# Performance work log

Hardware: AMD Instinct MI355X
Metric: run time of the kernel (lower is better)

Reference implementation:

```python
import jax, jax.numpy as jnp
import numpy as np
import math

B, S, D, H = 2, 2048, 1024, 16
DK = D // H


def setup_inputs() -> dict:
    key = jax.random.key(0)
    ks = jax.random.split(key, 11)
    f = jnp.float32
    return {
        "query": jax.random.normal(ks[0], (B, S, D), f),
        "key": jax.random.normal(ks[1], (B, S, D), f),
        "value": jax.random.normal(ks[2], (B, S, D), f),
        "wq": jax.random.normal(ks[3], (D, D), f) * 0.02,
        "bq": jnp.zeros((D,), f),
        "wk": jax.random.normal(ks[4], (D, D), f) * 0.02,
        "bk": jnp.zeros((D,), f),
        "wv": jax.random.normal(ks[5], (D, D), f) * 0.02,
        "bv": jnp.zeros((D,), f),
        "wo": jax.random.normal(ks[6], (D, D), f) * 0.02,
        "bo": jnp.zeros((D,), f),
    }


def reference(query, key, value, wq, bq, wk, bk, wv, bv, wo, bo):
    # Linear projections (torch Linear: y = x @ W.T + b)
    q = query @ wq.T + bq
    k = key @ wk.T + bk
    v = value @ wv.T + bv
    # [B,S,D] -> [B,H,S,DK]
    q = q.reshape(B, S, H, DK).transpose(0, 2, 1, 3)
    k = k.reshape(B, S, H, DK).transpose(0, 2, 1, 3)
    v = v.reshape(B, S, H, DK).transpose(0, 2, 1, 3)
    scores = jnp.einsum("bhqd,bhkd->bhqk", q, k) / math.sqrt(DK)
    causal = jnp.triu(jnp.ones((S, S), dtype=bool), k=1)  # strict upper triangle masked
    scores = jnp.where(causal, -jnp.inf, scores)
    attn = jax.nn.softmax(scores, axis=-1)  # dropout is identity in eval (p=0)
    x = jnp.einsum("bhqk,bhkd->bhqd", attn, v)
    x = x.transpose(0, 2, 1, 3).reshape(B, S, D)
    return x @ wo.T + bo
```

## Files before the change

### kernel.cpp

```cpp
#include <hip/hip_runtime.h>
#include <math.h>

#define BB 2
#define SS 2048
#define DD 1024
#define HH 16
#define DKK 64
#define MM (BB * SS)
#define KK DD
#define VSTR 2176

typedef __attribute__((ext_vector_type(8))) short short8;
typedef __attribute__((ext_vector_type(4))) float floatx4;

__device__ inline unsigned short f2bf(float x) {
    unsigned int u = __float_as_uint(x);
    u += 0x7fffu + ((u >> 16) & 1u);
    return (unsigned short)(u >> 16);
}

__device__ inline unsigned int pkbf(float a, float b) {
    return (__float_as_uint(b) & 0xffff0000u) | (__float_as_uint(a) >> 16);
}

__device__ inline void cast4f(const float* __restrict__ in, unsigned short* __restrict__ out, int i) {
    const float4 v = *(const float4*)(in + i);
    unsigned long long pk = (unsigned long long)f2bf(v.x)
                          | ((unsigned long long)f2bf(v.y) << 16)
                          | ((unsigned long long)f2bf(v.z) << 32)
                          | ((unsigned long long)f2bf(v.w) << 48);
    *(unsigned long long*)(out + i) = pk;
}

__global__ __launch_bounds__(256) void cast_all(const float* __restrict__ q, const float* __restrict__ k,
                                                const float* __restrict__ v,
                                                const float* __restrict__ wq, const float* __restrict__ wk,
                                                const float* __restrict__ wv, const float* __restrict__ wo,
                                                unsigned short* __restrict__ oq, unsigned short* __restrict__ ok,
                                                unsigned short* __restrict__ ov,
                                                unsigned short* __restrict__ owq, unsigned short* __restrict__ owk,
                                                unsigned short* __restrict__ owv, unsigned short* __restrict__ owo) {
    const int blk = blockIdx.x;
    const float* in;
    unsigned short* out;
    int idx;
    if (blk < 12288) {
        const int w = blk >> 12;
        idx = blk & 4095;
        in  = (w == 0) ? q : (w == 1) ? k : v;
        out = (w == 0) ? oq : (w == 1) ? ok : ov;
    } else {
        const int w = (blk - 12288) >> 10;
        idx = (blk - 12288) & 1023;
        in  = (w == 0) ? wq : (w == 1) ? wk : (w == 2) ? wv : wo;
        out = (w == 0) ? owq : (w == 1) ? owk : (w == 2) ? owv : owo;
    }
    cast4f(in, out, (idx * 256 + threadIdx.x) * 4);
}

#define GLDS(gp, lp) __builtin_amdgcn_global_load_lds( \
    (const __attribute__((address_space(1))) void*)(gp), \
    (__attribute__((address_space(3))) void*)(lp), 16, 0, 0)

#define SCHED0() __builtin_amdgcn_sched_barrier(0)
#define BAR()    __builtin_amdgcn_s_barrier()
#define WAITL0() asm volatile("s_waitcnt lgkmcnt(0)" ::: "memory")
#define WAITV(n) asm volatile("s_waitcnt vmcnt(" #n ")" ::: "memory")

template<int MT>
__device__ __forceinline__ void gemm_mainloop(const unsigned short* __restrict__ A,
                                              const unsigned short* __restrict__ W,
                                              int m0, int n0,
                                              unsigned short* __restrict__ As,
                                              unsigned short* __restrict__ Bs,
                                              floatx4 (&acc)[MT * 4][4]) {
    const int t    = threadIdx.x;
    const int lane = t & 63;
    const int wave = t >> 6;
    const int col  = lane & 15;
    const int quad = lane >> 4;
    const int wr   = wave >> 2;
    const int wc   = wave & 3;
    const int wm   = wr * (MT * 64);
    const int wn   = wc * 64;

    const int r   = t >> 3;
    const int cs  = t & 7;
    const int ksw = (cs ^ (r & 7)) * 8;

    const int sA0 = (quad ^ (col & 7)) * 8;
    const int sA1 = ((quad + 4) ^ (col & 7)) * 8;

    auto stage = [&](int kt, int pb) {
        const int k0 = kt * 64;
        #pragma unroll
        for (int g = 0; g < 2 * MT; ++g)
            GLDS(A + (size_t)(m0 + g * 64 + r) * KK + k0 + ksw,
                 &As[pb * (MT * 128 * 64) + (g * 64 + r) * 64 + cs * 8]);
        #pragma unroll
        for (int g = 0; g < 4; ++g)
            GLDS(W + (size_t)(n0 + g * 64 + r) * KK + k0 + ksw,
                 &Bs[pb * (256 * 64) + (g * 64 + r) * 64 + cs * 8]);
    };

    stage(0, 0);
    stage(1, 1);
    if constexpr (MT == 2) { WAITV(8); } else { WAITV(6); }
    SCHED0(); BAR(); SCHED0();

    const int NK = KK / 64;
    for (int kt = 0; kt < NK; ++kt) {
        const int p = kt & 1;
        const unsigned short* Ab = &As[p * (MT * 128 * 64)];
        const unsigned short* Bb = &Bs[p * (256 * 64)];

        short8 a0[MT * 4], a1[MT * 4], b0[4], b1[4];
        #pragma unroll
        for (int i = 0; i < MT * 4; ++i) {
            const unsigned short* ar = Ab + (wm + i * 16 + col) * 64;
            a0[i] = *(const short8*)(ar + sA0);
            a1[i] = *(const short8*)(ar + sA1);
        }
        #pragma unroll
        for (int j = 0; j < 4; ++j) {
            const unsigned short* br = Bb + (wn + j * 16 + col) * 64;
            b0[j] = *(const short8*)(br + sA0);
            b1[j] = *(const short8*)(br + sA1);
        }

        #pragma unroll
        for (int i = 0; i < MT * 4; ++i)
            #pragma unroll
            for (int j = 0; j < 4; ++j)
                acc[i][j] = __builtin_amdgcn_mfma_f32_16x16x32_bf16(a0[i], b0[j], acc[i][j], 0, 0, 0);

        WAITL0(); SCHED0();
        BAR(); SCHED0();

        if (kt + 2 < NK) stage(kt + 2, p);

        __builtin_amdgcn_s_setprio(1);
        #pragma unroll
        for (int i = 0; i < MT * 4; ++i)
            #pragma unroll
            for (int j = 0; j < 4; ++j)
                acc[i][j] = __builtin_amdgcn_mfma_f32_16x16x32_bf16(a1[i], b1[j], acc[i][j], 0, 0, 0);
        __builtin_amdgcn_s_setprio(0);

        if (kt + 2 < NK) {
            if constexpr (MT == 2) { WAITV(8); } else { WAITV(6); }
        } else {
            WAITV(0);
        }
        SCHED0(); BAR(); SCHED0();
    }
}

__global__ __launch_bounds__(512, 2) void gemm_qkv(const unsigned short* __restrict__ qB,
                                                   const unsigned short* __restrict__ kB,
                                                   const unsigned short* __restrict__ vB,
                                                   const unsigned short* __restrict__ wqB,
                                                   const unsigned short* __restrict__ wkB,
                                                   const unsigned short* __restrict__ wvB,
                                                   const float* __restrict__ bq,
                                                   const float* __restrict__ bk,
                                                   const float* __restrict__ bv,
                                                   unsigned short* __restrict__ Qh,
                                                   unsigned short* __restrict__ Kh,
                                                   unsigned short* __restrict__ Vt) {
    __shared__ __align__(16) unsigned short As[2 * 256 * 64];
    __shared__ __align__(16) unsigned short Bs[2 * 256 * 64];

    const int bid   = blockIdx.x;
    const int wgid  = (bid & 7) * 24 + (bid >> 3);
    const int which = wgid >> 6;
    const int tile  = wgid & 63;
    const int m0    = (tile & 15) * 256;
    const int n0    = (tile >> 4) * 256;

    const unsigned short* A = (which == 0) ? qB : (which == 1) ? kB : vB;
    const unsigned short* W = (which == 0) ? wqB : (which == 1) ? wkB : wvB;
    const float* bias       = (which == 0) ? bq : (which == 1) ? bk : bv;

    floatx4 acc[8][4] = {};
    gemm_mainloop<2>(A, W, m0, n0, As, Bs, acc);

    const int t    = threadIdx.x;
    const int lane = t & 63;
    const int wave = t >> 6;
    const int col  = lane & 15;
    const int quad = lane >> 4;
    const int wm   = (wave >> 2) * 128;
    const int wn   = (wave & 3) * 64;

    #pragma unroll
    for (int i = 0; i < 8; ++i) {
        #pragma unroll
        for (int j = 0; j < 4; ++j) {
            const int n  = n0 + wn + j * 16 + col;
            const float bv0 = bias[n];
            const int h = n >> 6, dk = n & 63;
            const int mb  = m0 + wm + i * 16 + quad * 4;
            const int bdx = mb >> 11, s = mb & 2047;
            if (which != 2) {
                unsigned short* O = (which == 0) ? Qh : Kh;
                #pragma unroll
                for (int rr = 0; rr < 4; ++rr)
                    O[(((size_t)(bdx * HH + h)) * SS + (s + rr)) * DKK + dk] = f2bf(acc[i][j][rr] + bv0);
            } else {
                unsigned short* vp = Vt + (((size_t)(bdx * HH + h)) * DKK + dk) * VSTR + s;
                uint2 w;
                w.x = (unsigned int)f2bf(acc[i][j][0] + bv0) | ((unsigned int)f2bf(acc[i][j][1] + bv0) << 16);
                w.y = (unsigned int)f2bf(acc[i][j][2] + bv0) | ((unsigned int)f2bf(acc[i][j][3] + bv0) << 16);
                *(uint2*)vp = w;
            }
        }
    }
}

__global__ __launch_bounds__(512, 2) void gemm_out(const unsigned short* __restrict__ A,
                                                   const unsigned short* __restrict__ W,
                                                   const float* __restrict__ bias,
                                                   float* __restrict__ C) {
    __shared__ __align__(16) unsigned short As[2 * 128 * 64];
    __shared__ __align__(16) unsigned short Bs[2 * 256 * 64];

    const int bid  = blockIdx.x;
    const int wgid = (bid & 7) * 16 + (bid >> 3);
    const int m0   = (wgid & 31) * 128;
    const int n0   = (wgid >> 5) * 256;

    floatx4 acc[4][4] = {};
    gemm_mainloop<1>(A, W, m0, n0, As, Bs, acc);

    const int t    = threadIdx.x;
    const int lane = t & 63;
    const int wave = t >> 6;
    const int col  = lane & 15;
    const int quad = lane >> 4;
    const int wm   = (wave >> 2) * 64;
    const int wn   = (wave & 3) * 64;

    #pragma unroll
    for (int i = 0; i < 4; ++i) {
        #pragma unroll
        for (int j = 0; j < 4; ++j) {
            const int n = n0 + wn + j * 16 + col;
            const float bv0 = bias[n];
            #pragma unroll
            for (int rr = 0; rr < 4; ++rr) {
                const int m = m0 + wm + i * 16 + quad * 4 + rr;
                C[(size_t)m * DD + n] = acc[i][j][rr] + bv0;
            }
        }
    }
}

#define C1 0.18033688011112042f
#define C2 11.541560327111707f
#define MFMA __builtin_amdgcn_mfma_f32_16x16x32_bf16

__global__ __launch_bounds__(512) void attn_mfma(const unsigned short* __restrict__ Qh,
                                                 const unsigned short* __restrict__ Kh,
                                                 const unsigned short* __restrict__ Vt,
                                                 unsigned short* __restrict__ X) {
    __shared__ __align__(16) unsigned short Ks[2][64 * 64];
    __shared__ __align__(16) unsigned short Vs[2][64 * 64];
    __shared__ __align__(16) unsigned short Plds[8][16 * 40];

    const int t    = threadIdx.x;
    const int lane = t & 63;
    const int wave = t >> 6;
    const int col  = lane & 15;
    const int quad = lane >> 4;

    const int lin = blockIdx.x;
    const int bh  = (lin & 7) + 8 * ((lin >> 3) & 3);
    const int pr  = lin >> 5;
    const int b   = bh / HH, h = bh % HH;

    const int cX  = (wave < 4) ? (31 - pr) : pr;
    const int q0  = cX * 64 + (wave & 3) * 16;
    const int nst = 32 - pr;

    const unsigned short* Kb = Kh + (size_t)bh * SS * DKK;
    const unsigned short* Vb = Vt + (size_t)bh * DKK * VSTR;

    const int r0  = t >> 3;
    const int sg0 = ((t & 7) ^ (r0 & 7)) * 8;

    unsigned short* Pw = &Plds[wave][0];

    const unsigned short* Qb = Qh + ((size_t)bh * SS + q0) * DKK;
    const short8 qa0 = *(const short8*)(Qb + (size_t)col * DKK + quad * 8);
    const short8 qa1 = *(const short8*)(Qb + (size_t)col * DKK + 32 + quad * 8);

    floatx4 o0 = {0.f, 0.f, 0.f, 0.f}, o1 = o0, o2 = o0, o3 = o0;
    float lp = 0.f;

    const int ksA = ((quad)      ^ (col & 7)) * 8;
    const int ksB = ((quad | 4)  ^ (col & 7)) * 8;

    GLDS(Kb + (size_t)r0 * DKK + sg0,  &Ks[0][t * 8]);
    GLDS(Vb + (size_t)r0 * VSTR + sg0, &Vs[0][t * 8]);

    int cur = 0;
    for (int kb = 0; kb < nst; ++kb) {
        __syncthreads();

        if (kb + 1 < nst) {
            const int jn = (kb + 1) * 64;
            const int nx = cur ^ 1;
            GLDS(Kb + (size_t)(jn + r0) * DKK + sg0,  &Ks[nx][t * 8]);
            GLDS(Vb + (size_t)r0 * VSTR + jn + sg0,   &Vs[nx][t * 8]);
        }

        const unsigned short* Kp = &Ks[cur][0];
        const unsigned short* Vp = &Vs[cur][0];

        #pragma unroll
        for (int hh = 0; hh < 2; ++hh) {
            const int j0 = kb * 64 + hh * 32;
            if (j0 < q0 + 16) {
                const short8 k0 = *(const short8*)(Kp + (hh * 32 + col) * 64 + ksA);
                const short8 k1 = *(const short8*)(Kp + (hh * 32 + col) * 64 + ksB);
                const short8 k2 = *(const short8*)(Kp + (hh * 32 + col + 16) * 64 + ksA);
                const short8 k3 = *(const short8*)(Kp + (hh * 32 + col + 16) * 64 + ksB);

                floatx4 t0 = {0.f, 0.f, 0.f, 0.f}, t1 = t0;
                __builtin_amdgcn_s_setprio(1);
                t0 = MFMA(k0, qa0, t0, 0, 0, 0);
                t0 = MFMA(k1, qa1, t0, 0, 0, 0);
                t1 = MFMA(k2, qa0, t1, 0, 0, 0);
                t1 = MFMA(k3, qa1, t1, 0, 0, 0);
                __builtin_amdgcn_s_setprio(0);

                float p[8];
                if (j0 + 31 > q0) {
                    const int lim = q0 + col - j0;
                    #pragma unroll
                    for (int r = 0; r < 4; ++r) {
                        p[r]     = (quad * 4 + r      <= lim) ? __builtin_exp2f(fmaf(t0[r], C1, -C2)) : 0.f;
                        p[4 + r] = (16 + quad * 4 + r <= lim) ? __builtin_exp2f(fmaf(t1[r], C1, -C2)) : 0.f;
                    }
                } else {
                    #pragma unroll
                    for (int r = 0; r < 4; ++r) {
                        p[r]     = __builtin_exp2f(fmaf(t0[r], C1, -C2));
                        p[4 + r] = __builtin_exp2f(fmaf(t1[r], C1, -C2));
                    }
                }
                lp += (p[0] + p[1]) + (p[2] + p[3]) + (p[4] + p[5]) + (p[6] + p[7]);

                uint2 w0 = { pkbf(p[0], p[1]), pkbf(p[2], p[3]) };
                uint2 w1 = { pkbf(p[4], p[5]), pkbf(p[6], p[7]) };
                *(uint2*)(Pw + col * 40 + quad * 4)      = w0;
                *(uint2*)(Pw + col * 40 + 16 + quad * 4) = w1;

                const short8 pb = *(const short8*)(Pw + col * 40 + quad * 8);
                const int vs = hh ? ksB : ksA;
                const short8 v0 = *(const short8*)(Vp + (col)      * 64 + vs);
                const short8 v1 = *(const short8*)(Vp + (col + 16) * 64 + vs);
                const short8 v2 = *(const short8*)(Vp + (col + 32) * 64 + vs);
                const short8 v3 = *(const short8*)(Vp + (col + 48) * 64 + vs);
                __builtin_amdgcn_s_setprio(1);
                o0 = MFMA(v0, pb, o0, 0, 0, 0);
                o1 = MFMA(v1, pb, o1, 0, 0, 0);
                o2 = MFMA(v2, pb, o2, 0, 0, 0);
                o3 = MFMA(v3, pb, o3, 0, 0, 0);
                __builtin_amdgcn_s_setprio(0);
            }
        }

        cur ^= 1;
    }

    lp += __shfl_xor(lp, 16, 64);
    lp += __shfl_xor(lp, 32, 64);
    const float li = 1.f / lp;

    unsigned short* Xp = X + ((size_t)(b * SS + q0 + col)) * DD + h * DKK + quad * 4;
    {
        uint2 w;
        w.x = (unsigned int)f2bf(o0[0] * li) | ((unsigned int)f2bf(o0[1] * li) << 16);
        w.y = (unsigned int)f2bf(o0[2] * li) | ((unsigned int)f2bf(o0[3] * li) << 16);
        *(uint2*)(Xp + 0) = w;
        w.x = (unsigned int)f2bf(o1[0] * li) | ((unsigned int)f2bf(o1[1] * li) << 16);
        w.y = (unsigned int)f2bf(o1[2] * li) | ((unsigned int)f2bf(o1[3] * li) << 16);
        *(uint2*)(Xp + 16) = w;
        w.x = (unsigned int)f2bf(o2[0] * li) | ((unsigned int)f2bf(o2[1] * li) << 16);
        w.y = (unsigned int)f2bf(o2[2] * li) | ((unsigned int)f2bf(o2[3] * li) << 16);
        *(uint2*)(Xp + 32) = w;
        w.x = (unsigned int)f2bf(o3[0] * li) | ((unsigned int)f2bf(o3[1] * li) << 16);
        w.y = (unsigned int)f2bf(o3[2] * li) | ((unsigned int)f2bf(o3[3] * li) << 16);
        *(uint2*)(Xp + 48) = w;
    }
}

extern "C" void kernel_launch(void* const* d_in, const int* in_sizes, int n_in,
                              void* d_out, int out_size, void* d_ws, size_t ws_size,
                              hipStream_t stream) {
    const float* query = (const float*)d_in[0];
    const float* key   = (const float*)d_in[1];
    const float* value = (const float*)d_in[2];
    const float* wq    = (const float*)d_in[3];
    const float* bq    = (const float*)d_in[4];
    const float* wk    = (const float*)d_in[5];
    const float* bk    = (const float*)d_in[6];
    const float* wv    = (const float*)d_in[7];
    const float* bv    = (const float*)d_in[8];
    const float* wo    = (const float*)d_in[9];
    const float* bo    = (const float*)d_in[10];

    char* ws = (char*)d_ws;
    const size_t MB = 1024 * 1024;
    unsigned short* qB  = (unsigned short*)(ws);
    unsigned short* kB  = (unsigned short*)(ws + 8 * MB);
    unsigned short* vB  = (unsigned short*)(ws + 16 * MB);
    unsigned short* wqB = (unsigned short*)(ws + 24 * MB);
    unsigned short* wkB = (unsigned short*)(ws + 26 * MB);
    unsigned short* wvB = (unsigned short*)(ws + 28 * MB);
    unsigned short* woB = (unsigned short*)(ws + 30 * MB);
    unsigned short* Qh  = (unsigned short*)(ws + 32 * MB);
    unsigned short* Kh  = (unsigned short*)(ws + 40 * MB);
    unsigned short* Vt  = (unsigned short*)(ws + 48 * MB);
    unsigned short* Xb  = qB;

    cast_all<<<16384, 256, 0, stream>>>(query, key, value, wq, wk, wv, wo,
                                        qB, kB, vB, wqB, wkB, wvB, woB);

    gemm_qkv<<<192, 512, 0, stream>>>(qB, kB, vB, wqB, wkB, wvB, bq, bk, bv, Qh, Kh, Vt);

    attn_mfma<<<512, 512, 0, stream>>>(Qh, Kh, Vt, Xb);

    gemm_out<<<128, 512, 0, stream>>>(Xb, woB, bo, (float*)d_out);
}
```

Measured before the change: 219.2 us.

## Shrink GEMM tiles to 128x128 with 256-thread blocks and grid-stride cast

Replaces the 256x256 / 128x256 GEMM tiles with a uniform 128x128 tile run by 4 waves, raising block counts (768 for QKV, 256 for output) to fill more CUs. The pipeline changes from a two-stage-ahead prefetch with a mid-iteration barrier to a single prefetch per iteration followed by a full vmcnt(0) wait. The cast kernel becomes a grid-stride loop with 8 items per thread over 2048 blocks. Smaller tiles lower per-block operand reuse and the simpler pipeline may expose more load latency.

```diff
diff --git a/kernel.cpp b/kernel.cpp
--- a/kernel.cpp
+++ b/kernel.cpp
@@ -40,22 +40,27 @@
                                                 unsigned short* __restrict__ ov,
                                                 unsigned short* __restrict__ owq, unsigned short* __restrict__ owk,
                                                 unsigned short* __restrict__ owv, unsigned short* __restrict__ owo) {
-    const int blk = blockIdx.x;
-    const float* in;
-    unsigned short* out;
-    int idx;
-    if (blk < 12288) {
-        const int w = blk >> 12;
-        idx = blk & 4095;
-        in  = (w == 0) ? q : (w == 1) ? k : v;
-        out = (w == 0) ? oq : (w == 1) ? ok : ov;
-    } else {
-        const int w = (blk - 12288) >> 10;
-        idx = (blk - 12288) & 1023;
-        in  = (w == 0) ? wq : (w == 1) ? wk : (w == 2) ? wv : wo;
-        out = (w == 0) ? owq : (w == 1) ? owk : (w == 2) ? owv : owo;
-    }
-    cast4f(in, out, (idx * 256 + threadIdx.x) * 4);
+    const int tid = blockIdx.x * 256 + threadIdx.x;
+    #pragma unroll
+    for (int it = 0; it < 8; ++it) {
+        const int g = tid + it * 524288;
+        const float* in;
+        unsigned short* out;
+        int idx;
+        if (g < 3145728) {
+            const int w = g >> 20;
+            idx = g & 1048575;
+            in  = (w == 0) ? q : (w == 1) ? k : v;
+            out = (w == 0) ? oq : (w == 1) ? ok : ov;
+        } else {
+            const int gw = g - 3145728;
+            const int w = gw >> 18;
+            idx = gw & 262143;
+            in  = (w == 0) ? wq : (w == 1) ? wk : (w == 2) ? wv : wo;
+            out = (w == 0) ? owq : (w == 1) ? owk : (w == 2) ? owv : owo;
+        }
+        cast4f(in, out, idx * 4);
+    }
 }
 
 #define GLDS(gp, lp) __builtin_amdgcn_global_load_lds( \
@@ -67,26 +72,22 @@
 #define WAITL0() asm volatile("s_waitcnt lgkmcnt(0)" ::: "memory")
 #define WAITV(n) asm volatile("s_waitcnt vmcnt(" #n ")" ::: "memory")
 
-template<int MT>
-__device__ __forceinline__ void gemm_mainloop(const unsigned short* __restrict__ A,
-                                              const unsigned short* __restrict__ W,
-                                              int m0, int n0,
-                                              unsigned short* __restrict__ As,
-                                              unsigned short* __restrict__ Bs,
-                                              floatx4 (&acc)[MT * 4][4]) {
+__device__ __forceinline__ void gemm128_body(const unsigned short* __restrict__ A,
+                                             const unsigned short* __restrict__ W,
+                                             int m0, int n0,
+                                             unsigned short* __restrict__ As,
+                                             unsigned short* __restrict__ Bs,
+                                             floatx4 (&acc)[4][4]) {
     const int t    = threadIdx.x;
     const int lane = t & 63;
     const int wave = t >> 6;
     const int col  = lane & 15;
     const int quad = lane >> 4;
-    const int wr   = wave >> 2;
-    const int wc   = wave & 3;
-    const int wm   = wr * (MT * 64);
-    const int wn   = wc * 64;
-
-    const int r   = t >> 3;
-    const int cs  = t & 7;
-    const int ksw = (cs ^ (r & 7)) * 8;
+    const int wm   = (wave >> 1) * 64;
+    const int wn   = (wave & 1) * 64;
+
+    const int r  = t >> 3;
+    const int cs = t & 7;
 
     const int sA0 = (quad ^ (col & 7)) * 8;
     const int sA1 = ((quad + 4) ^ (col & 7)) * 8;
@@ -94,29 +95,34 @@
     auto stage = [&](int kt, int pb) {
         const int k0 = kt * 64;
         #pragma unroll
-        for (int g = 0; g < 2 * MT; ++g)
-            GLDS(A + (size_t)(m0 + g * 64 + r) * KK + k0 + ksw,
-                 &As[pb * (MT * 128 * 64) + (g * 64 + r) * 64 + cs * 8]);
-        #pragma unroll
-        for (int g = 0; g < 4; ++g)
-            GLDS(W + (size_t)(n0 + g * 64 + r) * KK + k0 + ksw,
-                 &Bs[pb * (256 * 64) + (g * 64 + r) * 64 + cs * 8]);
+        for (int g = 0; g < 4; ++g) {
+            const int row = g * 32 + r;
+            const int ksw = (cs ^ (row & 7)) * 8;
+            GLDS(A + (size_t)(m0 + row) * KK + k0 + ksw,
+                 &As[pb * (128 * 64) + row * 64 + cs * 8]);
+        }
+        #pragma unroll
+        for (int g = 0; g < 4; ++g) {
+            const int row = g * 32 + r;
+            const int ksw = (cs ^ (row & 7)) * 8;
+            GLDS(W + (size_t)(n0 + row) * KK + k0 + ksw,
+                 &Bs[pb * (128 * 64) + row * 64 + cs * 8]);
+        }
     };
 
     stage(0, 0);
-    stage(1, 1);
-    if constexpr (MT == 2) { WAITV(8); } else { WAITV(6); }
-    SCHED0(); BAR(); SCHED0();
+    WAITV(0); SCHED0(); BAR(); SCHED0();
 
     const int NK = KK / 64;
     for (int kt = 0; kt < NK; ++kt) {
         const int p = kt & 1;
-        const unsigned short* Ab = &As[p * (MT * 128 * 64)];
-        const unsigned short* Bb = &Bs[p * (256 * 64)];
-
-        short8 a0[MT * 4], a1[MT * 4], b0[4], b1[4];
-        #pragma unroll
-        for (int i = 0; i < MT * 4; ++i) {
+        if (kt + 1 < NK) stage(kt + 1, p ^ 1);
+
+        const unsigned short* Ab = &As[p * (128 * 64)];
+        const unsigned short* Bb = &Bs[p * (128 * 64)];
+        short8 a0[4], a1[4], b0[4], b1[4];
+        #pragma unroll
+        for (int i = 0; i < 4; ++i) {
             const unsigned short* ar = Ab + (wm + i * 16 + col) * 64;
             a0[i] = *(const short8*)(ar + sA0);
             a1[i] = *(const short8*)(ar + sA1);
@@ -128,35 +134,26 @@
             b1[j] = *(const short8*)(br + sA1);
         }
 
-        #pragma unroll
-        for (int i = 0; i < MT * 4; ++i)
+        __builtin_amdgcn_s_setprio(1);
+        #pragma unroll
+        for (int i = 0; i < 4; ++i)
             #pragma unroll
             for (int j = 0; j < 4; ++j)
                 acc[i][j] = __builtin_amdgcn_mfma_f32_16x16x32_bf16(a0[i], b0[j], acc[i][j], 0, 0, 0);
-
-        WAITL0(); SCHED0();
-        BAR(); SCHED0();
-
-        if (kt + 2 < NK) stage(kt + 2, p);
-
-        __builtin_amdgcn_s_setprio(1);
-        #pragma unroll
-        for (int i = 0; i < MT * 4; ++i)
+        #pragma unroll
+        for (int i = 0; i < 4; ++i)
             #pragma unroll
             for (int j = 0; j < 4; ++j)
                 acc[i][j] = __builtin_amdgcn_mfma_f32_16x16x32_bf16(a1[i], b1[j], acc[i][j], 0, 0, 0);
         __builtin_amdgcn_s_setprio(0);
 
-        if (kt + 2 < NK) {
-            if constexpr (MT == 2) { WAITV(8); } else { WAITV(6); }
-        } else {
-            WAITV(0);
-        }
+        WAITL0(); SCHED0();
+        if (kt + 1 < NK) { WAITV(0); }
         SCHED0(); BAR(); SCHED0();
     }
 }
 
-__global__ __launch_bounds__(512, 2) void gemm_qkv(const unsigned short* __restrict__ qB,
+__global__ __launch_bounds__(256, 2) void gemm_qkv(const unsigned short* __restrict__ qB,
                                                    const unsigned short* __restrict__ kB,
                                                    const unsigned short* __restrict__ vB,
                                                    const unsigned short* __restrict__ wqB,
@@ -168,33 +165,33 @@
                                                    unsigned short* __restrict__ Qh,
                                                    unsigned short* __restrict__ Kh,
                                                    unsigned short* __restrict__ Vt) {
-    __shared__ __align__(16) unsigned short As[2 * 256 * 64];
-    __shared__ __align__(16) unsigned short Bs[2 * 256 * 64];
+    __shared__ __align__(16) unsigned short As[2 * 128 * 64];
+    __shared__ __align__(16) unsigned short Bs[2 * 128 * 64];
 
     const int bid   = blockIdx.x;
-    const int wgid  = (bid & 7) * 24 + (bid >> 3);
-    const int which = wgid >> 6;
-    const int tile  = wgid & 63;
-    const int m0    = (tile & 15) * 256;
-    const int n0    = (tile >> 4) * 256;
+    const int wgid  = (bid & 7) * 96 + (bid >> 3);
+    const int which = wgid >> 8;
+    const int tile  = wgid & 255;
+    const int m0    = (tile >> 3) * 128;
+    const int n0    = (tile & 7) * 128;
 
     const unsigned short* A = (which == 0) ? qB : (which == 1) ? kB : vB;
     const unsigned short* W = (which == 0) ? wqB : (which == 1) ? wkB : wvB;
     const float* bias       = (which == 0) ? bq : (which == 1) ? bk : bv;
 
-    floatx4 acc[8][4] = {};
-    gemm_mainloop<2>(A, W, m0, n0, As, Bs, acc);
+    floatx4 acc[4][4] = {};
+    gemm128_body(A, W, m0, n0, As, Bs, acc);
 
     const int t    = threadIdx.x;
     const int lane = t & 63;
     const int wave = t >> 6;
     const int col  = lane & 15;
     const int quad = lane >> 4;
-    const int wm   = (wave >> 2) * 128;
-    const int wn   = (wave & 3) * 64;
+    const int wm   = (wave >> 1) * 64;
+    const int wn   = (wave & 1) * 64;
 
     #pragma unroll
-    for (int i = 0; i < 8; ++i) {
+    for (int i = 0; i < 4; ++i) {
         #pragma unroll
         for (int j = 0; j < 4; ++j) {
             const int n  = n0 + wn + j * 16 + col;
@@ -218,28 +215,28 @@
     }
 }
 
-__global__ __launch_bounds__(512, 2) void gemm_out(const unsigned short* __restrict__ A,
+__global__ __launch_bounds__(256, 2) void gemm_out(const unsigned short* __restrict__ A,
                                                    const unsigned short* __restrict__ W,
                                                    const float* __restrict__ bias,
                                                    float* __restrict__ C) {
     __shared__ __align__(16) unsigned short As[2 * 128 * 64];
-    __shared__ __align__(16) unsigned short Bs[2 * 256 * 64];
+    __shared__ __align__(16) unsigned short Bs[2 * 128 * 64];
 
     const int bid  = blockIdx.x;
-    const int wgid = (bid & 7) * 16 + (bid >> 3);
-    const int m0   = (wgid & 31) * 128;
-    const int n0   = (wgid >> 5) * 256;
+    const int wgid = (bid & 7) * 32 + (bid >> 3);
+    const int m0   = (wgid >> 3) * 128;
+    const int n0   = (wgid & 7) * 128;
 
     floatx4 acc[4][4] = {};
-    gemm_mainloop<1>(A, W, m0, n0, As, Bs, acc);
+    gemm128_body(A, W, m0, n0, As, Bs, acc);
 
     const int t    = threadIdx.x;
     const int lane = t & 63;
     const int wave = t >> 6;
     const int col  = lane & 15;
     const int quad = lane >> 4;
-    const int wm   = (wave >> 2) * 64;
-    const int wn   = (wave & 3) * 64;
+    const int wm   = (wave >> 1) * 64;
+    const int wn   = (wave & 1) * 64;
 
     #pragma unroll
     for (int i = 0; i < 4; ++i) {
@@ -426,12 +423,12 @@
     unsigned short* Vt  = (unsigned short*)(ws + 48 * MB);
     unsigned short* Xb  = qB;
 
-    cast_all<<<16384, 256, 0, stream>>>(query, key, value, wq, wk, wv, wo,
-                                        qB, kB, vB, wqB, wkB, wvB, woB);
-
-    gemm_qkv<<<192, 512, 0, stream>>>(qB, kB, vB, wqB, wkB, wvB, bq, bk, bv, Qh, Kh, Vt);
+    cast_all<<<2048, 256, 0, stream>>>(query, key, value, wq, wk, wv, wo,
+                                       qB, kB, vB, wqB, wkB, wvB, woB);
+
+    gemm_qkv<<<768, 256, 0, stream>>>(qB, kB, vB, wqB, wkB, wvB, bq, bk, bv, Qh, Kh, Vt);
 
     attn_mfma<<<512, 512, 0, stream>>>(Qh, Kh, Vt, Xb);
 
-    gemm_out<<<128, 512, 0, stream>>>(Xb, woB, bo, (float*)d_out);
-}
+    gemm_out<<<256, 256, 0, stream>>>(Xb, woB, bo, (float*)d_out);
+}
```

New measurement: 219.8 us. Within noise of the previous version (+0.3%).
